# Performance work log

Hardware: AMD Instinct MI355X
Metric: run time of the kernel (lower is better)

The kernel has to match this reference:

```python
import jax, jax.numpy as jnp
import numpy as np

B, N, M_PARAM, F_IN, HEADS, HID, OUT, MLP_H, N_ACT = 64, 512, 50, 3, 2, 3, 3, 128, 512
NEG_SLOPE = 0.2


def setup_inputs() -> dict:
    key = jax.random.key(0)
    ks = jax.random.split(key, 20)
    s = 0.1
    idx = jax.random.uniform(ks[0], (B, N), dtype=jnp.float32)
    x = jax.random.normal(ks[1], (B, N, F_IN), dtype=jnp.float32)
    y = jax.random.normal(ks[2], (B, M_PARAM + 2, F_IN), dtype=jnp.float32)
    adj = (jax.random.uniform(ks[3], (B, N, N)) < 0.02).astype(jnp.float32)
    # GATConv 1: in=3 -> heads=2, out=3 (concat)
    W1 = jax.random.normal(ks[4], (F_IN, HEADS * HID), dtype=jnp.float32) * s
    a_src1 = jax.random.normal(ks[5], (HEADS, HID), dtype=jnp.float32) * s
    a_dst1 = jax.random.normal(ks[6], (HEADS, HID), dtype=jnp.float32) * s
    b1 = jnp.zeros((HEADS * HID,), dtype=jnp.float32)
    # GATConv 2: in=6 -> heads=1, out=3
    W2 = jax.random.normal(ks[7], (HEADS * HID, OUT), dtype=jnp.float32) * s
    a_src2 = jax.random.normal(ks[8], (1, OUT), dtype=jnp.float32) * s
    a_dst2 = jax.random.normal(ks[9], (1, OUT), dtype=jnp.float32) * s
    b2 = jnp.zeros((OUT,), dtype=jnp.float32)
    fc_in = N + N * OUT + (M_PARAM + 2) * 3  # 2204
    Wf1 = jax.random.normal(ks[10], (fc_in, MLP_H), dtype=jnp.float32) * (1.0 / np.sqrt(fc_in))
    bf1 = jnp.zeros((MLP_H,), dtype=jnp.float32)
    Wf2 = jax.random.normal(ks[11], (MLP_H, N_ACT), dtype=jnp.float32) * (1.0 / np.sqrt(MLP_H))
    bf2 = jnp.zeros((N_ACT,), dtype=jnp.float32)
    return {"idx": idx, "x": x, "y": y, "adj": adj,
            "W1": W1, "a_src1": a_src1, "a_dst1": a_dst1, "b1": b1,
            "W2": W2, "a_src2": a_src2, "a_dst2": a_dst2, "b2": b2,
            "Wf1": Wf1, "bf1": bf1, "Wf2": Wf2, "bf2": bf2}


def gat_layer(x, adj, W, a_src, a_dst, bias):
    # PyG GATConv (concat=True): h = x W; alpha_ij = softmax_i(leaky_relu(a_src.h_i + a_dst.h_j))
    # edge (i -> j) exists iff adj[i, j] != 0; self-loops added per PyG default.
    Bb, Nn = x.shape[0], x.shape[1]
    Hh, D = a_src.shape
    h = (x @ W).reshape(Bb, Nn, Hh, D)                     # [B,N,H,D]
    es = jnp.einsum('bnhd,hd->bnh', h, a_src)              # source term
    ed = jnp.einsum('bnhd,hd->bnh', h, a_dst)              # target term
    logits = es[:, :, None, :] + ed[:, None, :, :]         # [B, i(src), j(dst), H]
    logits = jax.nn.leaky_relu(logits, NEG_SLOPE)
    mask = (adj > 0) | jnp.eye(Nn, dtype=bool)[None]       # self-loops
    logits = jnp.where(mask[..., None], logits, jnp.float32(-1e9))
    alpha = jax.nn.softmax(logits, axis=1)                 # softmax over sources per target
    out = jnp.einsum('bijh,bihd->bjhd', alpha, h)          # aggregate at targets
    return out.reshape(Bb, Nn, Hh * D) + bias


def reference(idx, x, y, adj, W1, a_src1, a_dst1, b1, W2, a_src2, a_dst2, b2, Wf1, bf1, Wf2, bf2):
    g = jax.nn.relu(gat_layer(x, adj, W1, a_src1, a_dst1, b1))
    g = gat_layer(g, adj, W2, a_src2, a_dst2, b2)          # heads=1
    feat = jnp.concatenate([idx.reshape(B, -1), g.reshape(B, -1), y.reshape(B, -1)], axis=-1)
    h = jax.nn.relu(feat @ Wf1 + bf1)
    return h @ Wf2 + bf2
```

## Files before the change

kernel.cpp:

```cpp
#include <hip/hip_runtime.h>
#include <hip/hip_bf16.h>
#include <stdint.h>

#define B_    64
#define N_    512
#define M2    52
#define MLPH  128
#define NACT  512
#define FC_IN 2204
#define NCH   18
#define NEG   0.2f
#define NW    16

__device__ __forceinline__ float lrelu(float v){ return v > 0.f ? v : NEG * v; }

__global__ __launch_bounds__(512) void kfuse1(const float* __restrict__ adj,
                                              const float* __restrict__ x,
                                              const float* __restrict__ W1,
                                              const float* __restrict__ as1,
                                              const float* __restrict__ ad1,
                                              const float* __restrict__ b1,
                                              const float* __restrict__ W2,
                                              const float* __restrict__ as2,
                                              uint32_t* __restrict__ maskT,
                                              float* __restrict__ node2){
  __shared__ uint32_t lm[2][64][16];
  __shared__ float node[N_][8];
  int b  = blockIdx.y;
  int j0 = blockIdx.x * 64;
  int t  = threadIdx.x;

  {
    int j4 = t & 15;
    int w  = (t >> 4) & 15;
    int kh = t >> 8;
    const float* basef = adj + ((size_t)(b * N_ + (w << 5) + (kh << 4))) * N_ + (j0 + (j4 << 2));
    uint32_t m0 = 0, m1 = 0, m2 = 0, m3 = 0;
#pragma unroll
    for (int k = 0; k < 16; ++k) {
      float4 v = *(const float4*)(basef + (size_t)k * N_);
      m0 |= (v.x > 0.f ? 1u : 0u) << k;
      m1 |= (v.y > 0.f ? 1u : 0u) << k;
      m2 |= (v.z > 0.f ? 1u : 0u) << k;
      m3 |= (v.w > 0.f ? 1u : 0u) << k;
    }
    int sh = kh << 4;
    lm[kh][(j4 << 2) + 0][w] = m0 << sh;
    lm[kh][(j4 << 2) + 1][w] = m1 << sh;
    lm[kh][(j4 << 2) + 2][w] = m2 << sh;
    lm[kh][(j4 << 2) + 3][w] = m3 << sh;
  }

  {
    float xv0 = x[((size_t)(b * N_ + t)) * 3 + 0];
    float xv1 = x[((size_t)(b * N_ + t)) * 3 + 1];
    float xv2 = x[((size_t)(b * N_ + t)) * 3 + 2];
    float h[6];
#pragma unroll
    for (int c = 0; c < 6; ++c) h[c] = xv0 * W1[c] + xv1 * W1[6 + c] + xv2 * W1[12 + c];
#pragma unroll
    for (int c = 0; c < 6; ++c) node[t][c] = h[c];
    node[t][6] = h[0] * as1[0] + h[1] * as1[1] + h[2] * as1[2];
    node[t][7] = h[3] * as1[3] + h[4] * as1[4] + h[5] * as1[5];
  }
  __syncthreads();

  int w  = t & 15;
  int tg = t >> 4;
  float ad10 = ad1[0], ad11 = ad1[1], ad12 = ad1[2];
  float ad13 = ad1[3], ad14 = ad1[4], ad15 = ad1[5];
  float b10 = b1[0], b11 = b1[1], b12 = b1[2], b13 = b1[3], b14 = b1[4], b15 = b1[5];
  float as20 = as2[0], as21 = as2[1], as22 = as2[2];

#pragma unroll
  for (int p = 0; p < 2; ++p) {
    int jj = tg + p * 32;
    int j  = j0 + jj;
    uint32_t bits = lm[0][jj][w] | lm[1][jj][w];
    maskT[((size_t)(b * N_ + j)) * NW + w] = bits;
    if ((j >> 5) == w) bits |= 1u << (j & 31);

    float ed0 = node[j][0] * ad10 + node[j][1] * ad11 + node[j][2] * ad12;
    float ed1 = node[j][3] * ad13 + node[j][4] * ad14 + node[j][5] * ad15;

    float den0 = 0.f, den1 = 0.f;
    float a0 = 0.f, a1 = 0.f, a2 = 0.f, a3 = 0.f, a4 = 0.f, a5 = 0.f;
    while (bits) {
      int k = __ffs(bits) - 1;
      bits &= bits - 1;
      int i = (w << 5) + k;
      float e0 = __expf(lrelu(node[i][6] + ed0));
      float e1 = __expf(lrelu(node[i][7] + ed1));
      den0 += e0; den1 += e1;
      a0 += e0 * node[i][0]; a1 += e0 * node[i][1]; a2 += e0 * node[i][2];
      a3 += e1 * node[i][3]; a4 += e1 * node[i][4]; a5 += e1 * node[i][5];
    }
#pragma unroll
    for (int m = 1; m < 16; m <<= 1) {
      den0 += __shfl_xor(den0, m); den1 += __shfl_xor(den1, m);
      a0 += __shfl_xor(a0, m); a1 += __shfl_xor(a1, m); a2 += __shfl_xor(a2, m);
      a3 += __shfl_xor(a3, m); a4 += __shfl_xor(a4, m); a5 += __shfl_xor(a5, m);
    }
    float r0 = 1.f / den0, r1 = 1.f / den1;
    float g0 = fmaxf(a0 * r0 + b10, 0.f);
    float g1v = fmaxf(a1 * r0 + b11, 0.f);
    float g2v = fmaxf(a2 * r0 + b12, 0.f);
    float g3 = fmaxf(a3 * r1 + b13, 0.f);
    float g4 = fmaxf(a4 * r1 + b14, 0.f);
    float g5 = fmaxf(a5 * r1 + b15, 0.f);
    float h20 = g0*W2[0] + g1v*W2[3] + g2v*W2[6] + g3*W2[9]  + g4*W2[12] + g5*W2[15];
    float h21 = g0*W2[1] + g1v*W2[4] + g2v*W2[7] + g3*W2[10] + g4*W2[13] + g5*W2[16];
    float h22 = g0*W2[2] + g1v*W2[5] + g2v*W2[8] + g3*W2[11] + g4*W2[14] + g5*W2[17];
    float es2 = h20 * as20 + h21 * as21 + h22 * as22;
    if (w < 4) {
      float outv = (w == 0) ? h20 : (w == 1) ? h21 : (w == 2) ? h22 : es2;
      node2[((size_t)(b * N_ + j)) * 4 + w] = outv;
    }
  }
}

__global__ __launch_bounds__(256) void kagg2(const float* __restrict__ node2,
                                             const float* __restrict__ ad2,
                                             const float* __restrict__ b2,
                                             const uint32_t* __restrict__ maskT,
                                             float* __restrict__ g2){
  __shared__ float sn[N_][4];
  __shared__ uint32_t smq[128][NW];
  int q = blockIdx.x, b = blockIdx.y, t = threadIdx.x;

  const float4* nsrc = (const float4*)(node2 + (size_t)b * N_ * 4);
  const uint4*  msrc = (const uint4*)(maskT + ((size_t)b * N_ + q * 128) * NW);
  float4 nv0 = nsrc[t];
  float4 nv1 = nsrc[t + 256];
  uint4  mv0 = msrc[t];
  uint4  mv1 = msrc[t + 256];
  sn[t][0] = nv0.x; sn[t][1] = nv0.y; sn[t][2] = nv0.z; sn[t][3] = nv0.w;
  sn[t + 256][0] = nv1.x; sn[t + 256][1] = nv1.y; sn[t + 256][2] = nv1.z; sn[t + 256][3] = nv1.w;
  ((uint4*)smq)[t] = mv0;
  ((uint4*)smq)[t + 256] = mv1;
  __syncthreads();

  int w = t & 15, grp = t >> 4;
  float ad20 = ad2[0], ad21 = ad2[1], ad22 = ad2[2];
  float b20 = b2[0], b21 = b2[1], b22 = b2[2];
#pragma unroll
  for (int r = 0; r < 8; ++r) {
    int jl = r * 16 + grp;
    int j  = q * 128 + jl;
    uint32_t bits = smq[jl][w];
    if ((j >> 5) == w) bits |= 1u << (j & 31);
    float ed = sn[j][0] * ad20 + sn[j][1] * ad21 + sn[j][2] * ad22;
    float den = 0.f, a0 = 0.f, a1 = 0.f, a2 = 0.f;
    while (bits) {
      int k = __ffs(bits) - 1;
      bits &= bits - 1;
      int i = (w << 5) + k;
      float e = __expf(lrelu(sn[i][3] + ed));
      den += e;
      a0 += e * sn[i][0]; a1 += e * sn[i][1]; a2 += e * sn[i][2];
    }
#pragma unroll
    for (int m = 1; m < 16; m <<= 1) {
      den += __shfl_xor(den, m);
      a0 += __shfl_xor(a0, m); a1 += __shfl_xor(a1, m); a2 += __shfl_xor(a2, m);
    }
    if (w < 3) {
      float rr = 1.f / den;
      float v = (w == 0 ? a0 : w == 1 ? a1 : a2) * rr + (w == 0 ? b20 : w == 1 ? b21 : b22);
      g2[((size_t)(b * N_ + j)) * 3 + w] = v;
    }
  }
}

__global__ __launch_bounds__(256) void kmlp1v(const float* __restrict__ idx,
                                              const float* __restrict__ y,
                                              const float* __restrict__ g2,
                                              const float* __restrict__ Wf1,
                                              float* __restrict__ partial){
  __shared__ float fs[128];
  __shared__ float pr[8][128];
  int c = blockIdx.x, b = blockIdx.y, t = threadIdx.x;
  if (t < 128) {
    int k = c * 128 + t;
    float v = 0.f;
    if (k < N_)            v = idx[(size_t)b * N_ + k];
    else if (k < 2048)     v = g2[(size_t)b * (N_ * 3) + (k - N_)];
    else if (k < FC_IN)    v = y[(size_t)b * (M2 * 3) + (k - 2048)];
    fs[t] = v;
  }
  __syncthreads();

  int kq = t >> 5, ug = t & 31;
  const float4* wrow = (const float4*)(Wf1 + ((size_t)(c * 128 + kq * 16)) * MLPH) + ug;
  float a0 = 0.f, a1 = 0.f, a2 = 0.f, a3 = 0.f;
  if (c < 17) {
#pragma unroll
    for (int k2 = 0; k2 < 16; ++k2) {
      float fv = fs[kq * 16 + k2];
      float4 w = wrow[k2 * 32];
      a0 += fv * w.x; a1 += fv * w.y; a2 += fv * w.z; a3 += fv * w.w;
    }
  } else {
    int kend = min(16, (FC_IN - 17 * 128) - kq * 16);
    for (int k2 = 0; k2 < kend; ++k2) {
      float fv = fs[kq * 16 + k2];
      float4 w = wrow[k2 * 32];
      a0 += fv * w.x; a1 += fv * w.y; a2 += fv * w.z; a3 += fv * w.w;
    }
  }
  *(float4*)&pr[kq][ug * 4] = make_float4(a0, a1, a2, a3);
  __syncthreads();
  if (t < 128) {
    float s = 0.f;
#pragma unroll
    for (int q = 0; q < 8; ++q) s += pr[q][t];
    partial[((size_t)b * NCH + c) * MLPH + t] = s;
  }
}

__global__ __launch_bounds__(256) void kmlp2v(const float* __restrict__ partial,
                                              const float* __restrict__ bf1,
                                              const float* __restrict__ Wf2,
                                              const float* __restrict__ bf2,
                                              float* __restrict__ out){
  __shared__ float part[NCH * MLPH];
  __shared__ float hid[MLPH];
  __shared__ float pr[8][128];
  int q = blockIdx.x, b = blockIdx.y, t = threadIdx.x;

  const float4* src = (const float4*)(partial + (size_t)b * NCH * MLPH);
  float4 v0 = src[t];
  float4 v1 = src[t + 256];
  float4 v2 = (t < 64) ? src[t + 512] : make_float4(0.f, 0.f, 0.f, 0.f);
  ((float4*)part)[t] = v0;
  ((float4*)part)[t + 256] = v1;
  if (t < 64) ((float4*)part)[t + 512] = v2;
  __syncthreads();
  if (t < 128) {
    float s = bf1[t];
#pragma unroll
    for (int c2 = 0; c2 < NCH; ++c2) s += part[c2 * MLPH + t];
    hid[t] = fmaxf(s, 0.f);
  }
  __syncthreads();

  int kh = t >> 5, ug = t & 31;
  const float4* wrow = (const float4*)(Wf2 + (size_t)(kh * 16) * NACT + q * 128) + ug;
  float a0 = 0.f, a1 = 0.f, a2 = 0.f, a3 = 0.f;
#pragma unroll
  for (int k2 = 0; k2 < 16; ++k2) {
    float hv = hid[kh * 16 + k2];
    float4 w = wrow[k2 * 128];
    a0 += hv * w.x; a1 += hv * w.y; a2 += hv * w.z; a3 += hv * w.w;
  }
  *(float4*)&pr[kh][ug * 4] = make_float4(a0, a1, a2, a3);
  __syncthreads();
  if (t < 128) {
    float s = bf2[q * 128 + t];
#pragma unroll
    for (int h = 0; h < 8; ++h) s += pr[h][t];
    out[(size_t)b * NACT + q * 128 + t] = s;
  }
}

extern "C" void kernel_launch(void* const* d_in, const int* in_sizes, int n_in,
                              void* d_out, int out_size, void* d_ws, size_t ws_size,
                              hipStream_t stream) {
  const float* idx = (const float*)d_in[0];
  const float* x   = (const float*)d_in[1];
  const float* y   = (const float*)d_in[2];
  const float* adj = (const float*)d_in[3];
  const float* W1  = (const float*)d_in[4];
  const float* as1 = (const float*)d_in[5];
  const float* ad1 = (const float*)d_in[6];
  const float* b1  = (const float*)d_in[7];
  const float* W2  = (const float*)d_in[8];
  const float* as2 = (const float*)d_in[9];
  const float* ad2 = (const float*)d_in[10];
  const float* b2  = (const float*)d_in[11];
  const float* Wf1 = (const float*)d_in[12];
  const float* bf1 = (const float*)d_in[13];
  const float* Wf2 = (const float*)d_in[14];
  const float* bf2 = (const float*)d_in[15];
  float* out = (float*)d_out;

  uint8_t* ws = (uint8_t*)d_ws;
  uint32_t* maskT = (uint32_t*)ws;
  float* node2    = (float*)(ws + 2097152);
  float* g2       = (float*)(ws + 2097152 + 524288);
  float* partial  = (float*)(ws + 2097152 + 524288 + 393216);

  hipLaunchKernelGGL(kfuse1, dim3(8, B_),   dim3(512), 0, stream,
                     adj, x, W1, as1, ad1, b1, W2, as2, maskT, node2);
  hipLaunchKernelGGL(kagg2,  dim3(4, B_),   dim3(256), 0, stream,
                     node2, ad2, b2, maskT, g2);
  hipLaunchKernelGGL(kmlp1v, dim3(NCH, B_), dim3(256), 0, stream,
                     idx, y, g2, Wf1, partial);
  hipLaunchKernelGGL(kmlp2v, dim3(4, B_),   dim3(256), 0, stream,
                     partial, bf1, Wf2, bf2, out);
}
```

Baseline: 35.18 us.

## Fuse GAT layer-2 aggregation, MLP layers into one kernel with last-block ticket

Replaces the three back-end kernels (layer-2 aggregation, first MLP partial products, second MLP) with one kernel. Blocks that cover the g2 slice of the feature vector compute their own aggregation rows in shared memory before the Wf1 partial product. The last block per batch, found through an atomic ticket counter reset in kfuse1, reduces the partials and runs the second MLP. This removes two launches and the g2 round-trip through global memory. In exchange it adds threadfence plus atomic serialization and puts the final layer on a single block per batch.

```diff
diff --git a/kernel.cpp b/kernel.cpp
--- a/kernel.cpp
+++ b/kernel.cpp
@@ -23,12 +23,15 @@
                                               const float* __restrict__ W2,
                                               const float* __restrict__ as2,
                                               uint32_t* __restrict__ maskT,
-                                              float* __restrict__ node2){
+                                              float* __restrict__ node2,
+                                              uint32_t* __restrict__ cnt){
   __shared__ uint32_t lm[2][64][16];
   __shared__ float node[N_][8];
   int b  = blockIdx.y;
   int j0 = blockIdx.x * 64;
   int t  = threadIdx.x;
+
+  if (blockIdx.x == 0 && t == 0) cnt[b] = 0;
 
   {
     int j4 = t & 15;
@@ -119,147 +122,169 @@
   }
 }
 
-__global__ __launch_bounds__(256) void kagg2(const float* __restrict__ node2,
-                                             const float* __restrict__ ad2,
-                                             const float* __restrict__ b2,
-                                             const uint32_t* __restrict__ maskT,
-                                             float* __restrict__ g2){
-  __shared__ float sn[N_][4];
-  __shared__ uint32_t smq[128][NW];
-  int q = blockIdx.x, b = blockIdx.y, t = threadIdx.x;
-
-  const float4* nsrc = (const float4*)(node2 + (size_t)b * N_ * 4);
-  const uint4*  msrc = (const uint4*)(maskT + ((size_t)b * N_ + q * 128) * NW);
-  float4 nv0 = nsrc[t];
-  float4 nv1 = nsrc[t + 256];
-  uint4  mv0 = msrc[t];
-  uint4  mv1 = msrc[t + 256];
-  sn[t][0] = nv0.x; sn[t][1] = nv0.y; sn[t][2] = nv0.z; sn[t][3] = nv0.w;
-  sn[t + 256][0] = nv1.x; sn[t + 256][1] = nv1.y; sn[t + 256][2] = nv1.z; sn[t + 256][3] = nv1.w;
-  ((uint4*)smq)[t] = mv0;
-  ((uint4*)smq)[t + 256] = mv1;
-  __syncthreads();
-
-  int w = t & 15, grp = t >> 4;
-  float ad20 = ad2[0], ad21 = ad2[1], ad22 = ad2[2];
-  float b20 = b2[0], b21 = b2[1], b22 = b2[2];
-#pragma unroll
-  for (int r = 0; r < 8; ++r) {
-    int jl = r * 16 + grp;
-    int j  = q * 128 + jl;
-    uint32_t bits = smq[jl][w];
-    if ((j >> 5) == w) bits |= 1u << (j & 31);
-    float ed = sn[j][0] * ad20 + sn[j][1] * ad21 + sn[j][2] * ad22;
-    float den = 0.f, a0 = 0.f, a1 = 0.f, a2 = 0.f;
-    while (bits) {
-      int k = __ffs(bits) - 1;
-      bits &= bits - 1;
-      int i = (w << 5) + k;
-      float e = __expf(lrelu(sn[i][3] + ed));
-      den += e;
-      a0 += e * sn[i][0]; a1 += e * sn[i][1]; a2 += e * sn[i][2];
-    }
-#pragma unroll
-    for (int m = 1; m < 16; m <<= 1) {
-      den += __shfl_xor(den, m);
-      a0 += __shfl_xor(a0, m); a1 += __shfl_xor(a1, m); a2 += __shfl_xor(a2, m);
-    }
-    if (w < 3) {
-      float rr = 1.f / den;
-      float v = (w == 0 ? a0 : w == 1 ? a1 : a2) * rr + (w == 0 ? b20 : w == 1 ? b21 : b22);
-      g2[((size_t)(b * N_ + j)) * 3 + w] = v;
-    }
-  }
-}
-
-__global__ __launch_bounds__(256) void kmlp1v(const float* __restrict__ idx,
+__global__ __launch_bounds__(256) void kback2(const float* __restrict__ idx,
                                               const float* __restrict__ y,
-                                              const float* __restrict__ g2,
+                                              const float* __restrict__ node2,
+                                              const float* __restrict__ ad2,
+                                              const float* __restrict__ b2,
+                                              const uint32_t* __restrict__ maskT,
                                               const float* __restrict__ Wf1,
-                                              float* __restrict__ partial){
-  __shared__ float fs[128];
-  __shared__ float pr[8][128];
-  int c = blockIdx.x, b = blockIdx.y, t = threadIdx.x;
-  if (t < 128) {
-    int k = c * 128 + t;
-    float v = 0.f;
-    if (k < N_)            v = idx[(size_t)b * N_ + k];
-    else if (k < 2048)     v = g2[(size_t)b * (N_ * 3) + (k - N_)];
-    else if (k < FC_IN)    v = y[(size_t)b * (M2 * 3) + (k - 2048)];
-    fs[t] = v;
-  }
-  __syncthreads();
-
-  int kq = t >> 5, ug = t & 31;
-  const float4* wrow = (const float4*)(Wf1 + ((size_t)(c * 128 + kq * 16)) * MLPH) + ug;
-  float a0 = 0.f, a1 = 0.f, a2 = 0.f, a3 = 0.f;
-  if (c < 17) {
-#pragma unroll
-    for (int k2 = 0; k2 < 16; ++k2) {
-      float fv = fs[kq * 16 + k2];
-      float4 w = wrow[k2 * 32];
-      a0 += fv * w.x; a1 += fv * w.y; a2 += fv * w.z; a3 += fv * w.w;
-    }
-  } else {
-    int kend = min(16, (FC_IN - 17 * 128) - kq * 16);
-    for (int k2 = 0; k2 < kend; ++k2) {
-      float fv = fs[kq * 16 + k2];
-      float4 w = wrow[k2 * 32];
-      a0 += fv * w.x; a1 += fv * w.y; a2 += fv * w.z; a3 += fv * w.w;
-    }
-  }
-  *(float4*)&pr[kq][ug * 4] = make_float4(a0, a1, a2, a3);
-  __syncthreads();
-  if (t < 128) {
-    float s = 0.f;
-#pragma unroll
-    for (int q = 0; q < 8; ++q) s += pr[q][t];
-    partial[((size_t)b * NCH + c) * MLPH + t] = s;
-  }
-}
-
-__global__ __launch_bounds__(256) void kmlp2v(const float* __restrict__ partial,
                                               const float* __restrict__ bf1,
                                               const float* __restrict__ Wf2,
                                               const float* __restrict__ bf2,
+                                              float* __restrict__ partial,
+                                              uint32_t* __restrict__ cnt,
                                               float* __restrict__ out){
-  __shared__ float part[NCH * MLPH];
+  __shared__ float sn[N_][4];
+  __shared__ uint32_t smq[44][NW];
+  __shared__ float gloc[44][3];
+  __shared__ float fs[128];
+  __shared__ float pr[8][128];
+  __shared__ float spart[NCH * MLPH];
   __shared__ float hid[MLPH];
-  __shared__ float pr[8][128];
-  int q = blockIdx.x, b = blockIdx.y, t = threadIdx.x;
-
-  const float4* src = (const float4*)(partial + (size_t)b * NCH * MLPH);
-  float4 v0 = src[t];
-  float4 v1 = src[t + 256];
-  float4 v2 = (t < 64) ? src[t + 512] : make_float4(0.f, 0.f, 0.f, 0.f);
-  ((float4*)part)[t] = v0;
-  ((float4*)part)[t + 256] = v1;
-  if (t < 64) ((float4*)part)[t + 512] = v2;
+  __shared__ uint32_t ticket;
+  int c = blockIdx.x, b = blockIdx.y, t = threadIdx.x;
+
+  if (c >= 4 && c < 16) {
+    int kg0 = c * 128 - 512;
+    int j0n = kg0 / 3;
+    int j1n = (kg0 + 127) / 3;
+    int nrow = j1n - j0n + 1;
+    const float4* nsrc = (const float4*)(node2 + (size_t)b * N_ * 4);
+    const uint4*  msrc = (const uint4*)(maskT + ((size_t)b * N_ + j0n) * NW);
+    float4 n0 = nsrc[t];
+    float4 n1 = nsrc[t + 256];
+    uint4 mv = make_uint4(0u, 0u, 0u, 0u);
+    if (t < nrow * 4) mv = msrc[t];
+    sn[t][0] = n0.x; sn[t][1] = n0.y; sn[t][2] = n0.z; sn[t][3] = n0.w;
+    sn[t + 256][0] = n1.x; sn[t + 256][1] = n1.y; sn[t + 256][2] = n1.z; sn[t + 256][3] = n1.w;
+    if (t < nrow * 4) ((uint4*)smq)[t] = mv;
+    __syncthreads();
+
+    int w = t & 15, grp = t >> 4;
+    float ad20 = ad2[0], ad21 = ad2[1], ad22 = ad2[2];
+    float b20 = b2[0], b21 = b2[1], b22 = b2[2];
+#pragma unroll
+    for (int rr = 0; rr < 3; ++rr) {
+      int ji = grp + rr * 16;
+      if (ji < nrow) {
+        int j = j0n + ji;
+        uint32_t bits = smq[ji][w];
+        if ((j >> 5) == w) bits |= 1u << (j & 31);
+        float ed = sn[j][0] * ad20 + sn[j][1] * ad21 + sn[j][2] * ad22;
+        float den = 0.f, a0 = 0.f, a1 = 0.f, a2 = 0.f;
+        while (bits) {
+          int k = __ffs(bits) - 1;
+          bits &= bits - 1;
+          int i = (w << 5) + k;
+          float e = __expf(lrelu(sn[i][3] + ed));
+          den += e;
+          a0 += e * sn[i][0]; a1 += e * sn[i][1]; a2 += e * sn[i][2];
+        }
+#pragma unroll
+        for (int m = 1; m < 16; m <<= 1) {
+          den += __shfl_xor(den, m);
+          a0 += __shfl_xor(a0, m); a1 += __shfl_xor(a1, m); a2 += __shfl_xor(a2, m);
+        }
+        if (w < 3) {
+          float rinv = 1.f / den;
+          gloc[ji][w] = (w == 0 ? a0 : w == 1 ? a1 : a2) * rinv
+                      + (w == 0 ? b20 : w == 1 ? b21 : b22);
+        }
+      }
+    }
+    __syncthreads();
+    if (t < 128) {
+      int kg = kg0 + t;
+      int j = kg / 3, comp = kg - 3 * j;
+      fs[t] = gloc[j - j0n][comp];
+    }
+  } else {
+    if (t < 128) {
+      int k = c * 128 + t;
+      float v = 0.f;
+      if (k < N_)                      v = idx[(size_t)b * N_ + k];
+      else if (k >= 2048 && k < FC_IN) v = y[(size_t)b * (M2 * 3) + (k - 2048)];
+      fs[t] = v;
+    }
+  }
+  __syncthreads();
+
+  {
+    int kq = t >> 5, ug = t & 31;
+    const float4* wrow = (const float4*)(Wf1 + ((size_t)(c * 128 + kq * 16)) * MLPH) + ug;
+    float a0 = 0.f, a1 = 0.f, a2 = 0.f, a3 = 0.f;
+    if (c < 17) {
+#pragma unroll
+      for (int k2 = 0; k2 < 16; ++k2) {
+        float fv = fs[kq * 16 + k2];
+        float4 w = wrow[k2 * 32];
+        a0 += fv * w.x; a1 += fv * w.y; a2 += fv * w.z; a3 += fv * w.w;
+      }
+    } else {
+      int kend = min(16, (FC_IN - 17 * 128) - kq * 16);
+      for (int k2 = 0; k2 < kend; ++k2) {
+        float fv = fs[kq * 16 + k2];
+        float4 w = wrow[k2 * 32];
+        a0 += fv * w.x; a1 += fv * w.y; a2 += fv * w.z; a3 += fv * w.w;
+      }
+    }
+    *(float4*)&pr[kq][ug * 4] = make_float4(a0, a1, a2, a3);
+  }
   __syncthreads();
   if (t < 128) {
-    float s = bf1[t];
-#pragma unroll
-    for (int c2 = 0; c2 < NCH; ++c2) s += part[c2 * MLPH + t];
-    hid[t] = fmaxf(s, 0.f);
-  }
-  __syncthreads();
-
-  int kh = t >> 5, ug = t & 31;
-  const float4* wrow = (const float4*)(Wf2 + (size_t)(kh * 16) * NACT + q * 128) + ug;
-  float a0 = 0.f, a1 = 0.f, a2 = 0.f, a3 = 0.f;
-#pragma unroll
-  for (int k2 = 0; k2 < 16; ++k2) {
-    float hv = hid[kh * 16 + k2];
-    float4 w = wrow[k2 * 128];
-    a0 += hv * w.x; a1 += hv * w.y; a2 += hv * w.z; a3 += hv * w.w;
-  }
-  *(float4*)&pr[kh][ug * 4] = make_float4(a0, a1, a2, a3);
-  __syncthreads();
-  if (t < 128) {
-    float s = bf2[q * 128 + t];
-#pragma unroll
-    for (int h = 0; h < 8; ++h) s += pr[h][t];
-    out[(size_t)b * NACT + q * 128 + t] = s;
+    float s = 0.f;
+#pragma unroll
+    for (int q = 0; q < 8; ++q) s += pr[q][t];
+    partial[((size_t)b * NCH + c) * MLPH + t] = s;
+  }
+  __syncthreads();
+  __threadfence();
+
+  if (t == 0) ticket = atomicAdd(&cnt[b], 1u);
+  __syncthreads();
+
+  if (ticket == NCH - 1) {
+    __threadfence();
+    const float4* psrc = (const float4*)(partial + (size_t)b * NCH * MLPH);
+    float4 p0 = psrc[t];
+    float4 p1 = psrc[t + 256];
+    float4 p2 = (t < 64) ? psrc[t + 512] : make_float4(0.f, 0.f, 0.f, 0.f);
+    ((float4*)spart)[t] = p0;
+    ((float4*)spart)[t + 256] = p1;
+    if (t < 64) ((float4*)spart)[t + 512] = p2;
+    __syncthreads();
+    if (t < MLPH) {
+      float s = bf1[t];
+#pragma unroll
+      for (int c2 = 0; c2 < NCH; ++c2) s += spart[c2 * MLPH + t];
+      hid[t] = fmaxf(s, 0.f);
+    }
+    __syncthreads();
+
+    int og = t & 127, kh = t >> 7;
+    const float4* W4 = (const float4*)Wf2;
+    float a0 = 0.f, a1 = 0.f, a2 = 0.f, a3 = 0.f;
+#pragma unroll 8
+    for (int k2 = 0; k2 < 64; ++k2) {
+      int kk = kh * 64 + k2;
+      float hv = hid[kk];
+      float4 w = W4[(size_t)kk * 128 + og];
+      a0 += hv * w.x; a1 += hv * w.y; a2 += hv * w.z; a3 += hv * w.w;
+    }
+    ((float4*)pr)[kh * 128 + og] = make_float4(a0, a1, a2, a3);
+    __syncthreads();
+    if (t < 128) {
+      float4 u = ((float4*)pr)[t];
+      float4 v = ((float4*)pr)[128 + t];
+      float4 bb = ((const float4*)bf2)[t];
+      float4 r;
+      r.x = u.x + v.x + bb.x;
+      r.y = u.y + v.y + bb.y;
+      r.z = u.z + v.z + bb.z;
+      r.w = u.w + v.w + bb.w;
+      ((float4*)(out + (size_t)b * NACT))[t] = r;
+    }
   }
 }
 
@@ -285,17 +310,14 @@
   float* out = (float*)d_out;
 
   uint8_t* ws = (uint8_t*)d_ws;
-  uint32_t* maskT = (uint32_t*)ws;
-  float* node2    = (float*)(ws + 2097152);
-  float* g2       = (float*)(ws + 2097152 + 524288);
-  float* partial  = (float*)(ws + 2097152 + 524288 + 393216);
-
-  hipLaunchKernelGGL(kfuse1, dim3(8, B_),   dim3(512), 0, stream,
-                     adj, x, W1, as1, ad1, b1, W2, as2, maskT, node2);
-  hipLaunchKernelGGL(kagg2,  dim3(4, B_),   dim3(256), 0, stream,
-                     node2, ad2, b2, maskT, g2);
-  hipLaunchKernelGGL(kmlp1v, dim3(NCH, B_), dim3(256), 0, stream,
-                     idx, y, g2, Wf1, partial);
-  hipLaunchKernelGGL(kmlp2v, dim3(4, B_),   dim3(256), 0, stream,
-                     partial, bf1, Wf2, bf2, out);
+  uint32_t* maskT   = (uint32_t*)ws;
+  float* node2      = (float*)(ws + 2097152);
+  float* partial    = (float*)(ws + 2097152 + 524288);
+  uint32_t* cnt     = (uint32_t*)(ws + 2097152 + 524288 + 589824);
+
+  hipLaunchKernelGGL(kfuse1, dim3(8, B_), dim3(512), 0, stream,
+                     adj, x, W1, as1, ad1, b1, W2, as2, maskT, node2, cnt);
+  hipLaunchKernelGGL(kback2, dim3(NCH, B_), dim3(256), 0, stream,
+                     idx, y, node2, ad2, b2, maskT, Wf1, bf1, Wf2, bf2,
+                     partial, cnt, out);
 }
```

New measurement: 123.9 us. +252.2%, slower.

## Fuse GAT layer-2 aggregation into first MLP partial-GEMV kernel

Applied to the files above, without the earlier changes.

Merges the second GAT aggregation kernel into the first MLP layer kernel. Each of the 12 chunks covering the g2 feature range now computes only the roughly 43 target nodes it needs, keeps them in shared memory, and feeds them straight into the Wf1 partial products. This removes one kernel launch and the g2 global round trip. In exchange, aggregation work is now packed into fewer blocks alongside the GEMV, and every such block reloads all of node2.

```diff
diff --git a/kernel.cpp b/kernel.cpp
--- a/kernel.cpp
+++ b/kernel.cpp
@@ -119,96 +119,107 @@
   }
 }
 
-__global__ __launch_bounds__(256) void kagg2(const float* __restrict__ node2,
-                                             const float* __restrict__ ad2,
-                                             const float* __restrict__ b2,
-                                             const uint32_t* __restrict__ maskT,
-                                             float* __restrict__ g2){
+__global__ __launch_bounds__(256) void kmid(const float* __restrict__ idx,
+                                            const float* __restrict__ y,
+                                            const float* __restrict__ node2,
+                                            const float* __restrict__ ad2,
+                                            const float* __restrict__ b2,
+                                            const uint32_t* __restrict__ maskT,
+                                            const float* __restrict__ Wf1,
+                                            float* __restrict__ partial){
   __shared__ float sn[N_][4];
-  __shared__ uint32_t smq[128][NW];
-  int q = blockIdx.x, b = blockIdx.y, t = threadIdx.x;
-
-  const float4* nsrc = (const float4*)(node2 + (size_t)b * N_ * 4);
-  const uint4*  msrc = (const uint4*)(maskT + ((size_t)b * N_ + q * 128) * NW);
-  float4 nv0 = nsrc[t];
-  float4 nv1 = nsrc[t + 256];
-  uint4  mv0 = msrc[t];
-  uint4  mv1 = msrc[t + 256];
-  sn[t][0] = nv0.x; sn[t][1] = nv0.y; sn[t][2] = nv0.z; sn[t][3] = nv0.w;
-  sn[t + 256][0] = nv1.x; sn[t + 256][1] = nv1.y; sn[t + 256][2] = nv1.z; sn[t + 256][3] = nv1.w;
-  ((uint4*)smq)[t] = mv0;
-  ((uint4*)smq)[t + 256] = mv1;
-  __syncthreads();
-
-  int w = t & 15, grp = t >> 4;
-  float ad20 = ad2[0], ad21 = ad2[1], ad22 = ad2[2];
-  float b20 = b2[0], b21 = b2[1], b22 = b2[2];
-#pragma unroll
-  for (int r = 0; r < 8; ++r) {
-    int jl = r * 16 + grp;
-    int j  = q * 128 + jl;
-    uint32_t bits = smq[jl][w];
-    if ((j >> 5) == w) bits |= 1u << (j & 31);
-    float ed = sn[j][0] * ad20 + sn[j][1] * ad21 + sn[j][2] * ad22;
-    float den = 0.f, a0 = 0.f, a1 = 0.f, a2 = 0.f;
-    while (bits) {
-      int k = __ffs(bits) - 1;
-      bits &= bits - 1;
-      int i = (w << 5) + k;
-      float e = __expf(lrelu(sn[i][3] + ed));
-      den += e;
-      a0 += e * sn[i][0]; a1 += e * sn[i][1]; a2 += e * sn[i][2];
-    }
-#pragma unroll
-    for (int m = 1; m < 16; m <<= 1) {
-      den += __shfl_xor(den, m);
-      a0 += __shfl_xor(a0, m); a1 += __shfl_xor(a1, m); a2 += __shfl_xor(a2, m);
-    }
-    if (w < 3) {
-      float rr = 1.f / den;
-      float v = (w == 0 ? a0 : w == 1 ? a1 : a2) * rr + (w == 0 ? b20 : w == 1 ? b21 : b22);
-      g2[((size_t)(b * N_ + j)) * 3 + w] = v;
-    }
-  }
-}
-
-__global__ __launch_bounds__(256) void kmlp1v(const float* __restrict__ idx,
-                                              const float* __restrict__ y,
-                                              const float* __restrict__ g2,
-                                              const float* __restrict__ Wf1,
-                                              float* __restrict__ partial){
+  __shared__ uint32_t smq[44][NW];
+  __shared__ float gloc[44][3];
   __shared__ float fs[128];
   __shared__ float pr[8][128];
   int c = blockIdx.x, b = blockIdx.y, t = threadIdx.x;
-  if (t < 128) {
-    int k = c * 128 + t;
-    float v = 0.f;
-    if (k < N_)            v = idx[(size_t)b * N_ + k];
-    else if (k < 2048)     v = g2[(size_t)b * (N_ * 3) + (k - N_)];
-    else if (k < FC_IN)    v = y[(size_t)b * (M2 * 3) + (k - 2048)];
-    fs[t] = v;
-  }
-  __syncthreads();
-
-  int kq = t >> 5, ug = t & 31;
-  const float4* wrow = (const float4*)(Wf1 + ((size_t)(c * 128 + kq * 16)) * MLPH) + ug;
-  float a0 = 0.f, a1 = 0.f, a2 = 0.f, a3 = 0.f;
-  if (c < 17) {
-#pragma unroll
-    for (int k2 = 0; k2 < 16; ++k2) {
-      float fv = fs[kq * 16 + k2];
-      float4 w = wrow[k2 * 32];
-      a0 += fv * w.x; a1 += fv * w.y; a2 += fv * w.z; a3 += fv * w.w;
+
+  if (c >= 4 && c < 16) {
+    int kg0 = c * 128 - 512;
+    int j0n = kg0 / 3;
+    int j1n = (kg0 + 127) / 3;
+    int nrow = j1n - j0n + 1;
+    const float4* nsrc = (const float4*)(node2 + (size_t)b * N_ * 4);
+    const uint4*  msrc = (const uint4*)(maskT + ((size_t)b * N_ + j0n) * NW);
+    float4 n0 = nsrc[t];
+    float4 n1 = nsrc[t + 256];
+    uint4 mv = make_uint4(0u, 0u, 0u, 0u);
+    if (t < nrow * 4) mv = msrc[t];
+    sn[t][0] = n0.x; sn[t][1] = n0.y; sn[t][2] = n0.z; sn[t][3] = n0.w;
+    sn[t + 256][0] = n1.x; sn[t + 256][1] = n1.y; sn[t + 256][2] = n1.z; sn[t + 256][3] = n1.w;
+    if (t < nrow * 4) ((uint4*)smq)[t] = mv;
+    __syncthreads();
+
+    int w = t & 15, grp = t >> 4;
+    float ad20 = ad2[0], ad21 = ad2[1], ad22 = ad2[2];
+    float b20 = b2[0], b21 = b2[1], b22 = b2[2];
+#pragma unroll
+    for (int rr = 0; rr < 3; ++rr) {
+      int ji = grp + rr * 16;
+      if (ji < nrow) {
+        int j = j0n + ji;
+        uint32_t bits = smq[ji][w];
+        if ((j >> 5) == w) bits |= 1u << (j & 31);
+        float ed = sn[j][0] * ad20 + sn[j][1] * ad21 + sn[j][2] * ad22;
+        float den = 0.f, a0 = 0.f, a1 = 0.f, a2 = 0.f;
+        while (bits) {
+          int k = __ffs(bits) - 1;
+          bits &= bits - 1;
+          int i = (w << 5) + k;
+          float e = __expf(lrelu(sn[i][3] + ed));
+          den += e;
+          a0 += e * sn[i][0]; a1 += e * sn[i][1]; a2 += e * sn[i][2];
+        }
+#pragma unroll
+        for (int m = 1; m < 16; m <<= 1) {
+          den += __shfl_xor(den, m);
+          a0 += __shfl_xor(a0, m); a1 += __shfl_xor(a1, m); a2 += __shfl_xor(a2, m);
+        }
+        if (w < 3) {
+          float rinv = 1.f / den;
+          gloc[ji][w] = (w == 0 ? a0 : w == 1 ? a1 : a2) * rinv
+                      + (w == 0 ? b20 : w == 1 ? b21 : b22);
+        }
+      }
+    }
+    __syncthreads();
+    if (t < 128) {
+      int kg = kg0 + t;
+      int j = kg / 3, comp = kg - 3 * j;
+      fs[t] = gloc[j - j0n][comp];
     }
   } else {
-    int kend = min(16, (FC_IN - 17 * 128) - kq * 16);
-    for (int k2 = 0; k2 < kend; ++k2) {
-      float fv = fs[kq * 16 + k2];
-      float4 w = wrow[k2 * 32];
-      a0 += fv * w.x; a1 += fv * w.y; a2 += fv * w.z; a3 += fv * w.w;
-    }
-  }
-  *(float4*)&pr[kq][ug * 4] = make_float4(a0, a1, a2, a3);
+    if (t < 128) {
+      int k = c * 128 + t;
+      float v = 0.f;
+      if (k < N_)                      v = idx[(size_t)b * N_ + k];
+      else if (k >= 2048 && k < FC_IN) v = y[(size_t)b * (M2 * 3) + (k - 2048)];
+      fs[t] = v;
+    }
+  }
+  __syncthreads();
+
+  {
+    int kq = t >> 5, ug = t & 31;
+    const float4* wrow = (const float4*)(Wf1 + ((size_t)(c * 128 + kq * 16)) * MLPH) + ug;
+    float a0 = 0.f, a1 = 0.f, a2 = 0.f, a3 = 0.f;
+    if (c < 17) {
+#pragma unroll
+      for (int k2 = 0; k2 < 16; ++k2) {
+        float fv = fs[kq * 16 + k2];
+        float4 w = wrow[k2 * 32];
+        a0 += fv * w.x; a1 += fv * w.y; a2 += fv * w.z; a3 += fv * w.w;
+      }
+    } else {
+      int kend = min(16, (FC_IN - 17 * 128) - kq * 16);
+      for (int k2 = 0; k2 < kend; ++k2) {
+        float fv = fs[kq * 16 + k2];
+        float4 w = wrow[k2 * 32];
+        a0 += fv * w.x; a1 += fv * w.y; a2 += fv * w.z; a3 += fv * w.w;
+      }
+    }
+    *(float4*)&pr[kq][ug * 4] = make_float4(a0, a1, a2, a3);
+  }
   __syncthreads();
   if (t < 128) {
     float s = 0.f;
@@ -287,15 +298,12 @@
   uint8_t* ws = (uint8_t*)d_ws;
   uint32_t* maskT = (uint32_t*)ws;
   float* node2    = (float*)(ws + 2097152);
-  float* g2       = (float*)(ws + 2097152 + 524288);
-  float* partial  = (float*)(ws + 2097152 + 524288 + 393216);
+  float* partial  = (float*)(ws + 2097152 + 524288);
 
   hipLaunchKernelGGL(kfuse1, dim3(8, B_),   dim3(512), 0, stream,
                      adj, x, W1, as1, ad1, b1, W2, as2, maskT, node2);
-  hipLaunchKernelGGL(kagg2,  dim3(4, B_),   dim3(256), 0, stream,
-                     node2, ad2, b2, maskT, g2);
-  hipLaunchKernelGGL(kmlp1v, dim3(NCH, B_), dim3(256), 0, stream,
-                     idx, y, g2, Wf1, partial);
+  hipLaunchKernelGGL(kmid,   dim3(NCH, B_), dim3(256), 0, stream,
+                     idx, y, node2, ad2, b2, maskT, Wf1, partial);
   hipLaunchKernelGGL(kmlp2v, dim3(4, B_),   dim3(256), 0, stream,
                      partial, bf1, Wf2, bf2, out);
 }
```

Result: faster. 30.97 us (median of 2 runs) (-12.0%).
